# Kernel tuning notes

Hardware: AMD Instinct MI355X
Metric: run time of the kernel (lower is better)

## Reference

```python
import jax, jax.numpy as jnp
import numpy as np

B, P, D, F = 2048, 16, 1024, 512  # batch, n_prompt, dim, fusion_dim
S = 2 * P  # sequence length
H = D // 2  # classifier hidden
LN_EPS = 1e-5


def _ln_relu(y, g, b):
    mu = jnp.mean(y, axis=-1, keepdims=True)
    var = jnp.mean(jnp.square(y - mu), axis=-1, keepdims=True)
    return jax.nn.relu((y - mu) * jax.lax.rsqrt(var + LN_EPS) * g + b)


def setup_inputs() -> dict:
    key = jax.random.key(0)
    ks = jax.random.split(key, 24)
    n = lambda k, shp, scale: jax.random.normal(k, shp, dtype=jnp.float32) * scale
    return {
        "q": n(ks[0], (B, S, D), 1.0),
        # nn.MultiheadAttention (1 head, batch_first)
        "in_proj_w": n(ks[1], (3 * D, D), 1.0 / np.sqrt(D)),
        "in_proj_b": jnp.zeros((3 * D,), jnp.float32),
        "out_w": n(ks[2], (D, D), 1.0 / np.sqrt(D)),
        "out_b": jnp.zeros((D,), jnp.float32),
        # 32 per-position classifiers, stacked: Linear(D,H)+ReLU+Linear(H,1)+ReLU
        "cls_w1": n(ks[3], (S, H, D), 1.0 / np.sqrt(D)),
        "cls_b1": jnp.zeros((S, H), jnp.float32),
        "cls_w2": n(ks[4], (S, H), 1.0 / np.sqrt(H)),
        "cls_b2": jnp.zeros((S,), jnp.float32),
        # fusion / projector heads: Linear(D,F)+LayerNorm(F)+ReLU
        "fus_w": n(ks[5], (F, D), 1.0 / np.sqrt(D)),
        "fus_b": jnp.zeros((F,), jnp.float32),
        "fus_g": jnp.ones((F,), jnp.float32),
        "fus_be": jnp.zeros((F,), jnp.float32),
        "pa_w": n(ks[6], (F, D), 1.0 / np.sqrt(D)),
        "pa_b": jnp.zeros((F,), jnp.float32),
        "pa_g": jnp.ones((F,), jnp.float32),
        "pa_be": jnp.zeros((F,), jnp.float32),
        "pv_w": n(ks[7], (F, D), 1.0 / np.sqrt(D)),
        "pv_b": jnp.zeros((F,), jnp.float32),
        "pv_g": jnp.ones((F,), jnp.float32),
        "pv_be": jnp.zeros((F,), jnp.float32),
    }


def reference(q, in_proj_w, in_proj_b, out_w, out_b,
              cls_w1, cls_b1, cls_w2, cls_b2,
              fus_w, fus_b, fus_g, fus_be,
              pa_w, pa_b, pa_g, pa_be,
              pv_w, pv_b, pv_g, pv_be):
    # --- single-head self-attention (nn.MultiheadAttention, eval mode) ---
    wq, wk, wv = jnp.split(in_proj_w, 3, axis=0)
    bq, bk, bv = jnp.split(in_proj_b, 3, axis=0)
    qp = jnp.einsum('bsd,ed->bse', q, wq) + bq
    kp = jnp.einsum('bsd,ed->bse', q, wk) + bk
    vp = jnp.einsum('bsd,ed->bse', q, wv) + bv
    scores = jnp.einsum('bse,bte->bst', qp, kp) / jnp.sqrt(jnp.float32(D))
    attn = jax.nn.softmax(scores, axis=-1)
    q_att = jnp.einsum('bst,bte->bse', attn, vp)
    q_att = jnp.einsum('bse,de->bsd', q_att, out_w) + out_b

    # --- per-position tiny classifiers, batched over the 32 slots ---
    h = jax.nn.relu(jnp.einsum('bsd,shd->bsh', q, cls_w1) + cls_b1)  # [B,S,H]
    d = jax.nn.relu(jnp.einsum('bsh,sh->bs', h, cls_w2) + cls_b2)    # [B,S]

    d_a = jax.nn.softmax(d[:, :P], axis=-1)
    d_v = jax.nn.softmax(d[:, P:], axis=-1)
    audio = jnp.einsum('bsd,bs->bd', q_att[:, :P, :], d_a)
    video = jnp.einsum('bsd,bs->bd', q_att[:, P:, :], d_v)
    fusion = (audio + video) * 0.5

    fusion_h = _ln_relu(fusion @ fus_w.T + fus_b, fus_g, fus_be)
    fusion_a = _ln_relu(audio @ pa_w.T + pa_b, pa_g, pa_be)
    fusion_v = _ln_relu(video @ pv_w.T + pv_b, pv_g, pv_be)
    return (fusion_h, fusion_a, fusion_v, d_a, d_v)
```

## Files before the change

### kernel.cpp

```cpp
#include <hip/hip_runtime.h>

#define Bdim 2048
#define Sdim 32
#define Ddim 1024
#define Fdim 512
#define Hdim 512

typedef __bf16 bf16_t;
typedef __bf16 bf16x8 __attribute__((ext_vector_type(8)));
typedef __bf16 bf16x4 __attribute__((ext_vector_type(4)));
typedef float  f32x4  __attribute__((ext_vector_type(4)));

#define BM 128
#define BN 128
#define BK 32

__device__ __forceinline__ void gll16(const bf16_t* g, bf16_t* l) {
  __builtin_amdgcn_global_load_lds((const __attribute__((address_space(1))) void*)g,
                                   (__attribute__((address_space(3))) void*)l,
                                   16, 0, 0);
}

__global__ void k_cvt_all(const float* __restrict__ q, const float* __restrict__ ipw,
                          const float* __restrict__ ow, const float* __restrict__ cw1,
                          const float* __restrict__ fusw, const float* __restrict__ paw,
                          const float* __restrict__ pvw,
                          bf16_t* __restrict__ q16, bf16_t* __restrict__ w16,
                          bf16_t* __restrict__ ow16, bf16_t* __restrict__ cls16,
                          bf16_t* __restrict__ hw16) {
  long v = (long)blockIdx.x * 256 + threadIdx.x;
  const float* s; bf16_t* d; long off;
  if (v < 16777216L)      { s = q;    d = q16;            off = 0; }
  else if (v < 17563648L) { s = ipw;  d = w16;            off = 16777216L; }
  else if (v < 17825792L) { s = ow;   d = ow16;           off = 17563648L; }
  else if (v < 22020096L) { s = cw1;  d = cls16;          off = 17825792L; }
  else if (v < 22151168L) { s = fusw; d = hw16;           off = 22020096L; }
  else if (v < 22282240L) { s = paw;  d = hw16 + 524288;  off = 22151168L; }
  else                    { s = pvw;  d = hw16 + 1048576; off = 22282240L; }
  long i = (v - off) * 4;
  float4 t = *(const float4*)(s + i);
  bf16x4 o;
  o[0] = (bf16_t)t.x; o[1] = (bf16_t)t.y; o[2] = (bf16_t)t.z; o[3] = (bf16_t)t.w;
  *(bf16x4*)(d + i) = o;
}

__global__ void k_bias_pre(const float* __restrict__ ipw, const float* __restrict__ ipb,
                           const float* __restrict__ ow, const float* __restrict__ ob,
                           float* __restrict__ u, float* __restrict__ w,
                           float* __restrict__ bp, float* __restrict__ c0) {
  int blk = blockIdx.x, tid = threadIdx.x;
  if (blk < 4) {
    int d = blk * 256 + tid;
    float acc = 0.f;
    for (int e = 0; e < Ddim; ++e) acc += ipw[(long)e * Ddim + d] * ipb[Ddim + e];
    u[d] = acc;
  } else if (blk < 8) {
    int d = (blk - 4) * 256 + tid;
    float acc = 0.f;
    for (int e = 0; e < Ddim; ++e) acc += ipw[(long)(Ddim + e) * Ddim + d] * ipb[e];
    w[d] = acc;
  } else if (blk < 136) {
    int o = (blk - 8) * 8 + (tid >> 5);
    int l = tid & 31;
    float acc = 0.f;
    for (int e = l; e < Ddim; e += 32) acc += ow[(long)o * Ddim + e] * ipb[2 * Ddim + e];
    #pragma unroll
    for (int m = 1; m < 32; m <<= 1) acc += __shfl_xor(acc, m);
    if (l == 0) bp[o] = acc + ob[o];
  } else {
    __shared__ float red[256];
    float acc = 0.f;
    for (int e = tid; e < Ddim; e += 256) acc += ipb[e] * ipb[Ddim + e];
    red[tid] = acc;
    __syncthreads();
    for (int off = 128; off; off >>= 1) {
      if (tid < off) red[tid] += red[tid + off];
      __syncthreads();
    }
    if (tid == 0) c0[0] = red[0];
  }
}

template<int AT, int BT>
__device__ __forceinline__ void gemm_tile(const bf16_t* __restrict__ A, long lda,
                                          const bf16_t* __restrict__ Bt, long ldb,
                                          long m0, long n0, int K,
                                          bf16_t* sa, bf16_t* sb, f32x4 acc[4][4]) {
  const int tid  = threadIdx.x;
  const int wave = tid >> 6;
  const int lane = tid & 63;
  const int quad = lane >> 4;
  const int l16  = lane & 15;
  const int wm = (wave & 1) * 64;
  const int wn = (wave >> 1) * 64;

  for (int kt = 0; kt < K; kt += BK) {
    __syncthreads();
    if constexpr (AT == 0) {
      #pragma unroll
      for (int r = 0; r < 2; ++r) {
        int L = r * 256 + tid;
        const bf16_t* g = A + (m0 + (L >> 2)) * lda + kt + (L & 3) * 8;
        gll16(g, sa + (long)(r * 256 + wave * 64) * 8);
      }
    } else {
      #pragma unroll
      for (int r = 0; r < 2; ++r) {
        int L = r * 256 + tid;
        int gk = L >> 4, gm = (L & 15) * 8;
        bf16x8 v = *(const bf16x8*)(A + (long)(kt + gk) * lda + m0 + gm);
        #pragma unroll
        for (int j = 0; j < 8; ++j) sa[(gm + j) * BK + gk] = v[j];
      }
    }
    if constexpr (BT == 0) {
      #pragma unroll
      for (int r = 0; r < 2; ++r) {
        int L = r * 256 + tid;
        const bf16_t* g = Bt + (n0 + (L >> 2)) * ldb + kt + (L & 3) * 8;
        gll16(g, sb + (long)(r * 256 + wave * 64) * 8);
      }
    } else {
      #pragma unroll
      for (int r = 0; r < 2; ++r) {
        int L = r * 256 + tid;
        int gk = L >> 4, gn = (L & 15) * 8;
        bf16x8 v = *(const bf16x8*)(Bt + (long)(kt + gk) * ldb + n0 + gn);
        #pragma unroll
        for (int j = 0; j < 8; ++j) sb[(gn + j) * BK + gk] = v[j];
      }
    }
    __syncthreads();
    bf16x8 af[4], bfr[4];
    #pragma unroll
    for (int i = 0; i < 4; ++i)
      af[i] = *(const bf16x8*)(sa + (wm + i * 16 + l16) * BK + quad * 8);
    #pragma unroll
    for (int j = 0; j < 4; ++j)
      bfr[j] = *(const bf16x8*)(sb + (wn + j * 16 + l16) * BK + quad * 8);
    #pragma unroll
    for (int i = 0; i < 4; ++i)
      #pragma unroll
      for (int j = 0; j < 4; ++j)
        acc[i][j] = __builtin_amdgcn_mfma_f32_16x16x32_bf16(bfr[j], af[i], acc[i][j], 0, 0, 0);
  }
}

template<int AT, int BT>
__global__ __launch_bounds__(256) void k_gemm_bf16(
    const bf16_t* __restrict__ A, long lda, long sAz,
    const bf16_t* __restrict__ Bt, long ldb, long sBz,
    bf16_t* __restrict__ C, long ldc, long sCz,
    const float* __restrict__ bias, int K) {
  __shared__ bf16_t sa[BM * BK];
  __shared__ bf16_t sb[BN * BK];
  long n0 = (long)blockIdx.x * BN;
  long m0 = (long)blockIdx.y * BM;
  long z  = blockIdx.z;
  const bf16_t* Az = A + z * sAz;
  const bf16_t* Bz = Bt + z * sBz;
  bf16_t* Cz = C + z * sCz;
  f32x4 acc[4][4];
  #pragma unroll
  for (int i = 0; i < 4; ++i)
    #pragma unroll
    for (int j = 0; j < 4; ++j) acc[i][j] = (f32x4){0.f, 0.f, 0.f, 0.f};
  gemm_tile<AT, BT>(Az, lda, Bz, ldb, m0, n0, K, sa, sb, acc);
  const int tid = threadIdx.x, wave = tid >> 6, lane = tid & 63;
  const int quad = lane >> 4, l16 = lane & 15;
  const int wm = (wave & 1) * 64, wn = (wave >> 1) * 64;
  #pragma unroll
  for (int i = 0; i < 4; ++i) {
    long row = m0 + wm + i * 16 + l16;
    #pragma unroll
    for (int j = 0; j < 4; ++j) {
      long col = n0 + wn + j * 16 + quad * 4;
      f32x4 b4 = bias ? *(const f32x4*)(bias + col) : (f32x4){0.f, 0.f, 0.f, 0.f};
      bf16x4 o;
      #pragma unroll
      for (int r = 0; r < 4; ++r) o[r] = (bf16_t)(acc[i][j][r] + b4[r]);
      *(bf16x4*)(Cz + row * ldc + col) = o;
    }
  }
}

__global__ __launch_bounds__(256) void k_gemm_f32(
    const bf16_t* __restrict__ A, long lda, long sAz,
    const bf16_t* __restrict__ Bt, long ldb, long sBz,
    float* __restrict__ C, long ldc, long sCz, int K) {
  __shared__ bf16_t sa[BM * BK];
  __shared__ bf16_t sb[BN * BK];
  long n0 = (long)blockIdx.x * BN;
  long m0 = (long)blockIdx.y * BM;
  long z  = blockIdx.z;
  const bf16_t* Az = A + z * sAz;
  const bf16_t* Bz = Bt + z * sBz;
  float* Cz = C + z * sCz;
  f32x4 acc[4][4];
  #pragma unroll
  for (int i = 0; i < 4; ++i)
    #pragma unroll
    for (int j = 0; j < 4; ++j) acc[i][j] = (f32x4){0.f, 0.f, 0.f, 0.f};
  gemm_tile<0, 0>(Az, lda, Bz, ldb, m0, n0, K, sa, sb, acc);
  const int tid = threadIdx.x, wave = tid >> 6, lane = tid & 63;
  const int quad = lane >> 4, l16 = lane & 15;
  const int wm = (wave & 1) * 64, wn = (wave >> 1) * 64;
  #pragma unroll
  for (int i = 0; i < 4; ++i) {
    long row = m0 + wm + i * 16 + l16;
    #pragma unroll
    for (int j = 0; j < 4; ++j) {
      long col = n0 + wn + j * 16 + quad * 4;
      *(f32x4*)(Cz + row * ldc + col) = acc[i][j];
    }
  }
}

__global__ __launch_bounds__(256, 2) void k_gemm_big(
    const bf16_t* __restrict__ A, const bf16_t* __restrict__ Bt,
    bf16_t* __restrict__ C) {
  __shared__ bf16_t sa[128 * 32];
  __shared__ bf16_t sb[256 * 32];
  const int tid = threadIdx.x, wave = tid >> 6, lane = tid & 63;
  const int quad = lane >> 4, l16 = lane & 15;
  int lin = blockIdx.y * 4 + blockIdx.x;
  int c = lin & 7, j0 = lin >> 3;
  long m0 = ((long)c * 64 + (j0 >> 2)) * 128;
  long n0 = (long)(j0 & 3) * 256;
  const int wm = (wave & 1) * 64;
  const int wn = (wave >> 1) * 128;
  f32x4 acc[4][8];
  #pragma unroll
  for (int i = 0; i < 4; ++i)
    #pragma unroll
    for (int j = 0; j < 8; ++j) acc[i][j] = (f32x4){0.f, 0.f, 0.f, 0.f};
  for (int kt = 0; kt < 1024; kt += 32) {
    __syncthreads();
    #pragma unroll
    for (int r = 0; r < 2; ++r) {
      int L = r * 256 + tid;
      gll16(A + (m0 + (L >> 2)) * 1024 + kt + (L & 3) * 8, sa + (long)(r * 256 + wave * 64) * 8);
    }
    #pragma unroll
    for (int r = 0; r < 4; ++r) {
      int L = r * 256 + tid;
      gll16(Bt + (n0 + (L >> 2)) * 1024 + kt + (L & 3) * 8, sb + (long)(r * 256 + wave * 64) * 8);
    }
    __syncthreads();
    bf16x8 af[4], bfr[8];
    #pragma unroll
    for (int i = 0; i < 4; ++i)
      af[i] = *(const bf16x8*)(sa + (wm + i * 16 + l16) * 32 + quad * 8);
    #pragma unroll
    for (int j = 0; j < 8; ++j)
      bfr[j] = *(const bf16x8*)(sb + (wn + j * 16 + l16) * 32 + quad * 8);
    #pragma unroll
    for (int i = 0; i < 4; ++i)
      #pragma unroll
      for (int j = 0; j < 8; ++j)
        acc[i][j] = __builtin_amdgcn_mfma_f32_16x16x32_bf16(bfr[j], af[i], acc[i][j], 0, 0, 0);
  }
  #pragma unroll
  for (int i = 0; i < 4; ++i) {
    long row = m0 + wm + i * 16 + l16;
    #pragma unroll
    for (int j = 0; j < 8; ++j) {
      long col = n0 + wn + j * 16 + quad * 4;
      bf16x4 o;
      #pragma unroll
      for (int r = 0; r < 4; ++r) o[r] = (bf16_t)(acc[i][j][r]);
      *(bf16x4*)(C + row * 1024 + col) = o;
    }
  }
}

__global__ __launch_bounds__(256) void k_gemm_cls(
    const bf16_t* __restrict__ q16, const bf16_t* __restrict__ w1,
    const float* __restrict__ b1, const float* __restrict__ w2,
    float* __restrict__ dsum) {
  __shared__ bf16_t sa[BM * BK];
  __shared__ bf16_t sb[BN * BK];
  int lin = ((int)blockIdx.z * 16 + blockIdx.y) * 4 + blockIdx.x;
  int c = lin & 7, j0 = lin >> 3;
  int p = c + 8 * (j0 >> 2);
  long n0 = (long)(j0 & 3) * BN;
  int s = p >> 4;
  long m0 = (long)(p & 15) * BM;
  const bf16_t* A  = q16 + (long)s * Ddim;
  const bf16_t* Bt = w1 + (long)s * Hdim * Ddim;
  f32x4 acc[4][4];
  #pragma unroll
  for (int i = 0; i < 4; ++i)
    #pragma unroll
    for (int j = 0; j < 4; ++j) acc[i][j] = (f32x4){0.f, 0.f, 0.f, 0.f};
  gemm_tile<0, 0>(A, (long)Sdim * Ddim, Bt, Ddim, m0, n0, Ddim, sa, sb, acc);
  const int tid = threadIdx.x, wave = tid >> 6, lane = tid & 63;
  const int quad = lane >> 4, l16 = lane & 15;
  const int wm = (wave & 1) * 64, wn = (wave >> 1) * 64;
  const float* b1s = b1 + (long)s * Hdim;
  const float* w2s = w2 + (long)s * Hdim;
  #pragma unroll
  for (int i = 0; i < 4; ++i) {
    float vsum = 0.f;
    #pragma unroll
    for (int j = 0; j < 4; ++j) {
      long col = n0 + wn + j * 16 + quad * 4;
      f32x4 b4 = *(const f32x4*)(b1s + col);
      f32x4 w4 = *(const f32x4*)(w2s + col);
      #pragma unroll
      for (int r = 0; r < 4; ++r)
        vsum += fmaxf(acc[i][j][r] + b4[r], 0.f) * w4[r];
    }
    vsum += __shfl_xor(vsum, 16);
    vsum += __shfl_xor(vsum, 32);
    if (lane < 16) {
      long row = m0 + wm + i * 16 + l16;
      atomicAdd(&dsum[row * Sdim + s], vsum);
    }
  }
}

__global__ void k_finalize_d(const float* __restrict__ dsum, const float* __restrict__ cb2,
                             float* __restrict__ daws, float* __restrict__ out_da,
                             float* __restrict__ out_dv) {
  int t = blockIdx.x * 256 + threadIdx.x;
  int b = t >> 5, s = t & 31;
  float v = fmaxf(dsum[t] + cb2[s], 0.f);
  float m = v;
  #pragma unroll
  for (int mask = 1; mask < 16; mask <<= 1) m = fmaxf(m, __shfl_xor(m, mask));
  float e = __expf(v - m);
  float sum = e;
  #pragma unroll
  for (int mask = 1; mask < 16; mask <<= 1) sum += __shfl_xor(sum, mask);
  float r = e / sum;
  daws[t] = r;
  if (s < 16) out_da[b * 16 + s] = r;
  else        out_dv[b * 16 + (s - 16)] = r;
}

#define QPAD 264
__global__ __launch_bounds__(256) void k_attn_pool(
    const bf16_t* __restrict__ q16, const bf16_t* __restrict__ G16,
    const float* __restrict__ daws, const float* __restrict__ u,
    const float* __restrict__ wv, const float* __restrict__ c0p,
    bf16_t* __restrict__ pooled) {
  __shared__ bf16_t qc[32 * QPAD];
  __shared__ bf16_t gc[32 * QPAD];
  __shared__ float sc[32][33];
  __shared__ float qup[32][8], qwp[32][8];
  __shared__ float quL[32], qwL[32], caL[32], cvL[32], daL[16], dvL[16];
  const int tid = threadIdx.x, wave = tid >> 6, lane = tid & 63;
  const int quad = lane >> 4, l16 = lane & 15;
  const long b = blockIdx.x;
  const bf16_t* qb = q16 + b * (Sdim * Ddim);
  const bf16_t* gb = G16 + b * (Sdim * Ddim);
  if (tid < 32) {
    float dval = daws[b * Sdim + tid];
    if (tid < 16) daL[tid] = dval; else dvL[tid - 16] = dval;
  }
  qup[tid >> 3][tid & 7] = 0.f;
  qwp[tid >> 3][tid & 7] = 0.f;
  const int ti = wave & 1, tj = wave >> 1;
  f32x4 acc = (f32x4){0.f, 0.f, 0.f, 0.f};
  for (int kc = 0; kc < Ddim; kc += 256) {
    __syncthreads();
    #pragma unroll
    for (int r = 0; r < 4; ++r) {
      int L = r * 256 + tid;
      int row = L >> 5, koff = (L & 31) * 8;
      *(bf16x8*)(qc + row * QPAD + koff) = *(const bf16x8*)(qb + (long)row * Ddim + kc + koff);
      *(bf16x8*)(gc + row * QPAD + koff) = *(const bf16x8*)(gb + (long)row * Ddim + kc + koff);
    }
    __syncthreads();
    #pragma unroll
    for (int kk = 0; kk < 8; ++kk) {
      bf16x8 a  = *(const bf16x8*)(gc + (ti * 16 + l16) * QPAD + kk * 32 + quad * 8);
      bf16x8 bb = *(const bf16x8*)(qc + (tj * 16 + l16) * QPAD + kk * 32 + quad * 8);
      acc = __builtin_amdgcn_mfma_f32_16x16x32_bf16(a, bb, acc, 0, 0, 0);
    }
    {
      int s2 = tid & 31, sl = tid >> 5;
      float pu = 0.f, pw = 0.f;
      const bf16_t* qrow = qc + s2 * QPAD + sl * 32;
      for (int k = 0; k < 32; ++k) {
        float qv = (float)qrow[k];
        pu += qv * u[kc + sl * 32 + k];
        pw += qv * wv[kc + sl * 32 + k];
      }
      qup[s2][sl] += pu;
      qwp[s2][sl] += pw;
    }
  }
  __syncthreads();
  if (tid < 32) {
    float a0 = 0.f, a1 = 0.f;
    for (int k = 0; k < 8; ++k) { a0 += qup[tid][k]; a1 += qwp[tid][k]; }
    quL[tid] = a0; qwL[tid] = a1;
  }
  __syncthreads();
  {
    float c00 = c0p[0];
    int col = tj * 16 + l16;
    #pragma unroll
    for (int r = 0; r < 4; ++r) {
      int row = ti * 16 + quad * 4 + r;
      sc[row][col] = (acc[r] + quL[row] + qwL[col] + c00) * 0.03125f;
    }
  }
  __syncthreads();
  if (tid < 32) {
    float mx = -1e30f;
    for (int t = 0; t < 32; ++t) mx = fmaxf(mx, sc[tid][t]);
    float sum = 0.f;
    for (int t = 0; t < 32; ++t) { float e = __expf(sc[tid][t] - mx); sc[tid][t] = e; sum += e; }
    float inv = 1.f / sum;
    for (int t = 0; t < 32; ++t) sc[tid][t] *= inv;
  }
  __syncthreads();
  if (tid < 32) {
    float a0 = 0.f, a1 = 0.f;
    for (int s2 = 0; s2 < 16; ++s2) a0 += daL[s2] * sc[s2][tid];
    for (int s2 = 0; s2 < 16; ++s2) a1 += dvL[s2] * sc[16 + s2][tid];
    caL[tid] = a0; cvL[tid] = a1;
  }
  __syncthreads();
  {
    int d0 = tid * 4;
    float ap[4] = {0.f, 0.f, 0.f, 0.f}, vp[4] = {0.f, 0.f, 0.f, 0.f};
    for (int t = 0; t < 32; ++t) {
      float ca = caL[t], cv = cvL[t];
      bf16x4 qv = *(const bf16x4*)(qb + (long)t * Ddim + d0);
      #pragma unroll
      for (int e = 0; e < 4; ++e) {
        float x = (float)qv[e];
        ap[e] += ca * x;
        vp[e] += cv * x;
      }
    }
    bf16x4 pf, pa, pv;
    #pragma unroll
    for (int e = 0; e < 4; ++e) {
      pf[e] = (bf16_t)(0.5f * (ap[e] + vp[e]));
      pa[e] = (bf16_t)ap[e];
      pv[e] = (bf16_t)vp[e];
    }
    *(bf16x4*)(pooled + b * 3072 + d0)        = pf;
    *(bf16x4*)(pooled + b * 3072 + 1024 + d0) = pa;
    *(bf16x4*)(pooled + b * 3072 + 2048 + d0) = pv;
  }
}

__global__ __launch_bounds__(256) void k_ln(
    const float* __restrict__ Y,
    const float* __restrict__ fb, const float* __restrict__ fg, const float* __restrict__ fbe,
    const float* __restrict__ ab, const float* __restrict__ ag, const float* __restrict__ abe,
    const float* __restrict__ vb, const float* __restrict__ vg, const float* __restrict__ vbe,
    float* __restrict__ out) {
  int wave = threadIdx.x >> 6, lane = threadIdx.x & 63;
  long row = (long)blockIdx.x * 4 + wave;
  int head = (int)(row >> 11);
  const float* bb = (head == 0) ? fb : (head == 1) ? ab : vb;
  const float* gg = (head == 0) ? fg : (head == 1) ? ag : vg;
  const float* be = (head == 0) ? fbe : (head == 1) ? abe : vbe;
  const float* y = Y + row * Fdim + lane * 8;
  float v[8];
  float s = 0.f;
  #pragma unroll
  for (int k = 0; k < 8; ++k) { v[k] = y[k] + bb[lane * 8 + k]; s += v[k]; }
  #pragma unroll
  for (int m = 1; m < 64; m <<= 1) s += __shfl_xor(s, m);
  float mu = s * (1.f / Fdim);
  float vs = 0.f;
  #pragma unroll
  for (int k = 0; k < 8; ++k) { float t = v[k] - mu; vs += t * t; }
  #pragma unroll
  for (int m = 1; m < 64; m <<= 1) vs += __shfl_xor(vs, m);
  float inv = rsqrtf(vs * (1.f / Fdim) + 1e-5f);
  float* o = out + row * Fdim + lane * 8;
  #pragma unroll
  for (int k = 0; k < 8; ++k) {
    float t = (v[k] - mu) * inv * gg[lane * 8 + k] + be[lane * 8 + k];
    o[k] = fmaxf(t, 0.f);
  }
}

extern "C" void kernel_launch(void* const* d_in, const int* in_sizes, int n_in,
                              void* d_out, int out_size, void* d_ws, size_t ws_size,
                              hipStream_t stream) {
  const float* q    = (const float*)d_in[0];
  const float* ipw  = (const float*)d_in[1];
  const float* ipb  = (const float*)d_in[2];
  const float* ow   = (const float*)d_in[3];
  const float* ob   = (const float*)d_in[4];
  const float* cw1  = (const float*)d_in[5];
  const float* cb1  = (const float*)d_in[6];
  const float* cw2  = (const float*)d_in[7];
  const float* cb2  = (const float*)d_in[8];
  const float* fusw = (const float*)d_in[9];
  const float* fusb = (const float*)d_in[10];
  const float* fusg = (const float*)d_in[11];
  const float* fusbe= (const float*)d_in[12];
  const float* paw  = (const float*)d_in[13];
  const float* pab  = (const float*)d_in[14];
  const float* pag  = (const float*)d_in[15];
  const float* pabe = (const float*)d_in[16];
  const float* pvw  = (const float*)d_in[17];
  const float* pvb  = (const float*)d_in[18];
  const float* pvg  = (const float*)d_in[19];
  const float* pvbe = (const float*)d_in[20];
  float* out = (float*)d_out;

  const size_t o_q16   = 0;
  const size_t o_w16   = 134217728;
  const size_t o_ow16  = 140509184;
  const size_t o_cls16 = 142606336;
  const size_t o_hw16  = 176160768;
  const size_t o_Mt    = 179306496;
  const size_t o_Nt    = 181403648;
  const size_t o_G16   = 183500800;
  const size_t o_pool  = 317718528;
  const size_t o_u     = 330301440;
  const size_t o_wv    = 330305536;
  const size_t o_bp    = 330309632;
  const size_t o_c0    = 330313728;
  const size_t o_dsum  = 330313984;
  const size_t o_daws  = 330576128;
  const size_t total   = 330838272;
  if (ws_size < total) return;

  char* ws = (char*)d_ws;
  bf16_t* q16   = (bf16_t*)(ws + o_q16);
  bf16_t* w16   = (bf16_t*)(ws + o_w16);
  bf16_t* Wq16  = w16;
  bf16_t* Wk16  = w16 + 1048576;
  bf16_t* Wv16  = w16 + 2097152;
  bf16_t* ow16  = (bf16_t*)(ws + o_ow16);
  bf16_t* cls16 = (bf16_t*)(ws + o_cls16);
  bf16_t* hw16  = (bf16_t*)(ws + o_hw16);
  bf16_t* Mt    = (bf16_t*)(ws + o_Mt);
  bf16_t* Nt    = (bf16_t*)(ws + o_Nt);
  bf16_t* G16   = (bf16_t*)(ws + o_G16);
  bf16_t* S116  = (bf16_t*)(ws + o_G16);
  float*  Yf    = (float*)(ws + o_G16 + 12582912);
  bf16_t* pool16= (bf16_t*)(ws + o_pool);
  float*  uf    = (float*)(ws + o_u);
  float*  wvf   = (float*)(ws + o_wv);
  float*  bpf   = (float*)(ws + o_bp);
  float*  c0f   = (float*)(ws + o_c0);
  float*  dsum  = (float*)(ws + o_dsum);
  float*  daws  = (float*)(ws + o_daws);

  k_cvt_all<<<dim3(87552), dim3(256), 0, stream>>>(
      q, ipw, ow, cw1, fusw, paw, pvw, q16, w16, ow16, cls16, hw16);

  k_bias_pre<<<dim3(137), dim3(256), 0, stream>>>(ipw, ipb, ow, ob, uf, wvf, bpf, c0f);

  k_gemm_bf16<1, 1><<<dim3(8, 8, 1), dim3(256), 0, stream>>>(
      Wk16, Ddim, 0, Wq16, Ddim, 0, Mt, Ddim, 0, nullptr, Ddim);

  k_gemm_bf16<0, 1><<<dim3(8, 8, 1), dim3(256), 0, stream>>>(
      ow16, Ddim, 0, Wv16, Ddim, 0, Nt, Ddim, 0, nullptr, Ddim);

  k_gemm_big<<<dim3(4, 512), dim3(256), 0, stream>>>(q16, Mt, G16);

  hipMemsetAsync(dsum, 0, (size_t)Bdim * Sdim * sizeof(float), stream);
  k_gemm_cls<<<dim3(4, 16, 32), dim3(256), 0, stream>>>(q16, cls16, cb1, cw2, dsum);

  k_finalize_d<<<dim3(256), dim3(256), 0, stream>>>(
      dsum, cb2, daws, out + 3145728, out + 3145728 + 32768);

  k_attn_pool<<<dim3(2048), dim3(256), 0, stream>>>(q16, G16, daws, uf, wvf, c0f, pool16);

  k_gemm_bf16<0, 0><<<dim3(8, 48, 1), dim3(256), 0, stream>>>(
      pool16, Ddim, 0, Nt, Ddim, 0, S116, Ddim, 0, bpf, Ddim);

  k_gemm_f32<<<dim3(4, 16, 3), dim3(256), 0, stream>>>(
      S116, 3L * Ddim, Ddim, hw16, Ddim, (long)Fdim * Ddim,
      Yf, Fdim, (long)Bdim * Fdim, Ddim);

  k_ln<<<dim3(1536), dim3(256), 0, stream>>>(
      Yf, fusb, fusg, fusbe, pab, pag, pabe, pvb, pvg, pvbe, out);
}
```

Before: 1.058 ms.

## Swizzle LDS tiles to avoid bank conflicts, widen big-GEMM K tile, vectorize dot loops

Applies an XOR swizzle to the shared-memory layout of the GEMM A/B tiles, on both the global_load_lds writes and the fragment reads, to cut LDS bank conflicts. Doubles the K tile of the large GEMM to 64, halving its barriers per unit of work at the cost of more LDS per block. Also vectorizes the q·u / q·w dot loop in the score kernel and adds unroll pragmas to the bias precompute loops. The extra LDS could reduce occupancy of the large GEMM.

```diff
diff --git a/kernel.cpp b/kernel.cpp
--- a/kernel.cpp
+++ b/kernel.cpp
@@ -19,6 +19,10 @@
   __builtin_amdgcn_global_load_lds((const __attribute__((address_space(1))) void*)g,
                                    (__attribute__((address_space(3))) void*)l,
                                    16, 0, 0);
+}
+
+__device__ __forceinline__ int swz32(int row, int k) {
+  return row * 32 + (((((k >> 3) ^ ((row >> 1) & 3))) << 3) | (k & 7));
 }
 
 __global__ void k_cvt_all(const float* __restrict__ q, const float* __restrict__ ipw,
@@ -52,17 +56,20 @@
   if (blk < 4) {
     int d = blk * 256 + tid;
     float acc = 0.f;
+    #pragma unroll 8
     for (int e = 0; e < Ddim; ++e) acc += ipw[(long)e * Ddim + d] * ipb[Ddim + e];
     u[d] = acc;
   } else if (blk < 8) {
     int d = (blk - 4) * 256 + tid;
     float acc = 0.f;
+    #pragma unroll 8
     for (int e = 0; e < Ddim; ++e) acc += ipw[(long)(Ddim + e) * Ddim + d] * ipb[e];
     w[d] = acc;
   } else if (blk < 136) {
     int o = (blk - 8) * 8 + (tid >> 5);
     int l = tid & 31;
     float acc = 0.f;
+    #pragma unroll 4
     for (int e = l; e < Ddim; e += 32) acc += ow[(long)o * Ddim + e] * ipb[2 * Ddim + e];
     #pragma unroll
     for (int m = 1; m < 32; m <<= 1) acc += __shfl_xor(acc, m);
@@ -100,8 +107,9 @@
       #pragma unroll
       for (int r = 0; r < 2; ++r) {
         int L = r * 256 + tid;
-        const bf16_t* g = A + (m0 + (L >> 2)) * lda + kt + (L & 3) * 8;
-        gll16(g, sa + (long)(r * 256 + wave * 64) * 8);
+        int row = L >> 2, cs = L & 3;
+        int csrc = cs ^ ((row >> 1) & 3);
+        gll16(A + (m0 + row) * lda + kt + csrc * 8, sa + (long)(r * 256 + wave * 64) * 8);
       }
     } else {
       #pragma unroll
@@ -110,15 +118,16 @@
         int gk = L >> 4, gm = (L & 15) * 8;
         bf16x8 v = *(const bf16x8*)(A + (long)(kt + gk) * lda + m0 + gm);
         #pragma unroll
-        for (int j = 0; j < 8; ++j) sa[(gm + j) * BK + gk] = v[j];
+        for (int j = 0; j < 8; ++j) sa[swz32(gm + j, gk)] = v[j];
       }
     }
     if constexpr (BT == 0) {
       #pragma unroll
       for (int r = 0; r < 2; ++r) {
         int L = r * 256 + tid;
-        const bf16_t* g = Bt + (n0 + (L >> 2)) * ldb + kt + (L & 3) * 8;
-        gll16(g, sb + (long)(r * 256 + wave * 64) * 8);
+        int row = L >> 2, cs = L & 3;
+        int csrc = cs ^ ((row >> 1) & 3);
+        gll16(Bt + (n0 + row) * ldb + kt + csrc * 8, sb + (long)(r * 256 + wave * 64) * 8);
       }
     } else {
       #pragma unroll
@@ -127,17 +136,21 @@
         int gk = L >> 4, gn = (L & 15) * 8;
         bf16x8 v = *(const bf16x8*)(Bt + (long)(kt + gk) * ldb + n0 + gn);
         #pragma unroll
-        for (int j = 0; j < 8; ++j) sb[(gn + j) * BK + gk] = v[j];
+        for (int j = 0; j < 8; ++j) sb[swz32(gn + j, gk)] = v[j];
       }
     }
     __syncthreads();
     bf16x8 af[4], bfr[4];
     #pragma unroll
-    for (int i = 0; i < 4; ++i)
-      af[i] = *(const bf16x8*)(sa + (wm + i * 16 + l16) * BK + quad * 8);
-    #pragma unroll
-    for (int j = 0; j < 4; ++j)
-      bfr[j] = *(const bf16x8*)(sb + (wn + j * 16 + l16) * BK + quad * 8);
+    for (int i = 0; i < 4; ++i) {
+      int row = wm + i * 16 + l16;
+      af[i] = *(const bf16x8*)(sa + row * 32 + ((quad ^ ((row >> 1) & 3)) << 3));
+    }
+    #pragma unroll
+    for (int j = 0; j < 4; ++j) {
+      int row = wn + j * 16 + l16;
+      bfr[j] = *(const bf16x8*)(sb + row * 32 + ((quad ^ ((row >> 1) & 3)) << 3));
+    }
     #pragma unroll
     for (int i = 0; i < 4; ++i)
       #pragma unroll
@@ -219,8 +232,8 @@
 __global__ __launch_bounds__(256, 2) void k_gemm_big(
     const bf16_t* __restrict__ A, const bf16_t* __restrict__ Bt,
     bf16_t* __restrict__ C) {
-  __shared__ bf16_t sa[128 * 32];
-  __shared__ bf16_t sb[256 * 32];
+  __shared__ bf16_t sa[128 * 64];
+  __shared__ bf16_t sb[256 * 64];
   const int tid = threadIdx.x, wave = tid >> 6, lane = tid & 63;
   const int quad = lane >> 4, l16 = lane & 15;
   int lin = blockIdx.y * 4 + blockIdx.x;
@@ -234,31 +247,44 @@
   for (int i = 0; i < 4; ++i)
     #pragma unroll
     for (int j = 0; j < 8; ++j) acc[i][j] = (f32x4){0.f, 0.f, 0.f, 0.f};
-  for (int kt = 0; kt < 1024; kt += 32) {
+  for (int kt = 0; kt < 1024; kt += 64) {
     __syncthreads();
-    #pragma unroll
-    for (int r = 0; r < 2; ++r) {
-      int L = r * 256 + tid;
-      gll16(A + (m0 + (L >> 2)) * 1024 + kt + (L & 3) * 8, sa + (long)(r * 256 + wave * 64) * 8);
-    }
     #pragma unroll
     for (int r = 0; r < 4; ++r) {
       int L = r * 256 + tid;
-      gll16(Bt + (n0 + (L >> 2)) * 1024 + kt + (L & 3) * 8, sb + (long)(r * 256 + wave * 64) * 8);
+      int row = L >> 3, cs = L & 7;
+      int csrc = cs ^ ((row >> 1) & 7);
+      gll16(A + (m0 + row) * 1024 + kt + csrc * 8, sa + (long)(r * 256 + wave * 64) * 8);
+    }
+    #pragma unroll
+    for (int r = 0; r < 8; ++r) {
+      int L = r * 256 + tid;
+      int row = L >> 3, cs = L & 7;
+      int csrc = cs ^ ((row >> 1) & 7);
+      gll16(Bt + (n0 + row) * 1024 + kt + csrc * 8, sb + (long)(r * 256 + wave * 64) * 8);
     }
     __syncthreads();
-    bf16x8 af[4], bfr[8];
-    #pragma unroll
-    for (int i = 0; i < 4; ++i)
-      af[i] = *(const bf16x8*)(sa + (wm + i * 16 + l16) * 32 + quad * 8);
-    #pragma unroll
-    for (int j = 0; j < 8; ++j)
-      bfr[j] = *(const bf16x8*)(sb + (wn + j * 16 + l16) * 32 + quad * 8);
-    #pragma unroll
-    for (int i = 0; i < 4; ++i)
-      #pragma unroll
-      for (int j = 0; j < 8; ++j)
-        acc[i][j] = __builtin_amdgcn_mfma_f32_16x16x32_bf16(bfr[j], af[i], acc[i][j], 0, 0, 0);
+    #pragma unroll
+    for (int h = 0; h < 2; ++h) {
+      bf16x8 af[4], bfr[8];
+      #pragma unroll
+      for (int i = 0; i < 4; ++i) {
+        int row = wm + i * 16 + l16;
+        int cc = h * 4 + quad;
+        af[i] = *(const bf16x8*)(sa + row * 64 + ((cc ^ ((row >> 1) & 7)) << 3));
+      }
+      #pragma unroll
+      for (int j = 0; j < 8; ++j) {
+        int row = wn + j * 16 + l16;
+        int cc = h * 4 + quad;
+        bfr[j] = *(const bf16x8*)(sb + row * 64 + ((cc ^ ((row >> 1) & 7)) << 3));
+      }
+      #pragma unroll
+      for (int i = 0; i < 4; ++i)
+        #pragma unroll
+        for (int j = 0; j < 8; ++j)
+          acc[i][j] = __builtin_amdgcn_mfma_f32_16x16x32_bf16(bfr[j], af[i], acc[i][j], 0, 0, 0);
+    }
   }
   #pragma unroll
   for (int i = 0; i < 4; ++i) {
@@ -383,10 +409,20 @@
       int s2 = tid & 31, sl = tid >> 5;
       float pu = 0.f, pw = 0.f;
       const bf16_t* qrow = qc + s2 * QPAD + sl * 32;
-      for (int k = 0; k < 32; ++k) {
-        float qv = (float)qrow[k];
-        pu += qv * u[kc + sl * 32 + k];
-        pw += qv * wv[kc + sl * 32 + k];
+      const float* ub = u + kc + sl * 32;
+      const float* wb = wv + kc + sl * 32;
+      #pragma unroll
+      for (int kb = 0; kb < 4; ++kb) {
+        bf16x8 qv = *(const bf16x8*)(qrow + kb * 8);
+        f32x4 u0 = *(const f32x4*)(ub + kb * 8);
+        f32x4 u1 = *(const f32x4*)(ub + kb * 8 + 4);
+        f32x4 w0 = *(const f32x4*)(wb + kb * 8);
+        f32x4 w1 = *(const f32x4*)(wb + kb * 8 + 4);
+        #pragma unroll
+        for (int e = 0; e < 4; ++e) {
+          pu += (float)qv[e] * u0[e] + (float)qv[e + 4] * u1[e];
+          pw += (float)qv[e] * w0[e] + (float)qv[e + 4] * w1[e];
+        }
       }
       qup[s2][sl] += pu;
       qwp[s2][sl] += pw;
```

After: 1.031 ms. 2.6% less time.
